# Optimization experiments

Measured on AMD Instinct MI355X. Metric: run time of the kernel, lower is better.

## Reference

```python
import jax, jax.numpy as jnp
import numpy as np

R = 0.15          # ball-query radius (module init arg r)
K = 32            # _MAX_NEIGHBOURS
B, N = 8, 4096


def _ball_query(pos, r, k):
    """Dense ball query. pos: [B,N,3] -> neighbor idx [B,N,K], sorted by distance.
    Slots with fewer than k in-radius neighbors are filled with the query's own
    index (self is always the first neighbor at distance 0), so their
    contribution to (f_i - f_j)^2 is exactly 0 -- matching torch-points-kernels'
    fill-with-first-neighbor behaviour."""
    d2 = jnp.sum((pos[:, :, None, :] - pos[:, None, :, :]) ** 2, axis=-1)  # [B,N,N]
    masked = jnp.where(d2 <= r * r, d2, jnp.inf)
    neg_vals, idx = jax.lax.top_k(-masked, k)          # ascending distance
    valid = neg_vals > -jnp.inf
    self_idx = jnp.arange(pos.shape[1])[None, :, None]
    return jnp.where(valid, idx, self_idx)             # [B,N,K]


def setup_inputs() -> dict:
    key = jax.random.key(0)
    k1, k2 = jax.random.split(key)
    pos = jax.random.uniform(k1, (B, N, 3), dtype=jnp.float32)
    f = jax.random.normal(k2, (B, N), dtype=jnp.float32)
    return {"pos": pos, "f": f}


def reference(pos, f):
    # neighbor indices are non-differentiable (torch gathers with long indices)
    nei_idx = jax.lax.stop_gradient(_ball_query(pos, R, K))      # [B,N,K]
    f_nei = jax.vmap(lambda fb, ib: fb[ib])(f, nei_idx)          # [B,N,K]
    variances = jnp.sum((f[:, :, None] - f_nei) ** 2, axis=-1)   # [B,N]
    return 0.5 * jnp.mean(variances)
```

## Files before the change

### kernel.cpp

```cpp
#include <hip/hip_runtime.h>


#define BQ_K 32
#define CAP 128
#define WPB 4
#define G 6
#define NC (G * G * G)
#define CMAX 64
#define CAPC 512
#define QMAX 64
#define NPTS 4096

__device__ __forceinline__ int cell_coord(float x) {
    int c = (int)(x * (float)G);
    return c < 0 ? 0 : (c > G - 1 ? G - 1 : c);
}

__device__ __forceinline__ float select_sum(float2 e0, float2 e1, int M,
                                            float r2) {
    if (M <= BQ_K) return e0.y + e1.y;
    float lo = 0.0f, hi = r2 * 1.000001f;
    #pragma unroll
    for (int it = 0; it < 12; ++it) {
        const float mid = 0.5f * (lo + hi);
        const int cnt = __popcll(__ballot(e0.x < mid)) +
                        __popcll(__ballot(e1.x < mid));
        if (cnt >= BQ_K) hi = mid; else lo = mid;
    }
    float s = 0.0f;
    if (e0.x < hi) s = e0.y;
    if (e1.x < hi) s += e1.y;
    return s;
}

__global__ void dl_scatter(const float* __restrict__ pos,
                           const float* __restrict__ f,
                           int* __restrict__ cnt, float4* __restrict__ buck,
                           int total) {
    const int t = blockIdx.x * blockDim.x + threadIdx.x;
    if (t >= total) return;
    const int b = t >> 12;
    const float x = pos[3 * (size_t)t + 0];
    const float y = pos[3 * (size_t)t + 1];
    const float z = pos[3 * (size_t)t + 2];
    const int c = (cell_coord(z) * G + cell_coord(y)) * G + cell_coord(x);
    const int cell = b * NC + c;
    const int slot = atomicAdd(&cnt[cell], 1);
    if (slot < CMAX)
        buck[(size_t)cell * CMAX + slot] = make_float4(x, y, z, f[t]);
}

__global__ __launch_bounds__(256) void dl_main(
    const int* __restrict__ cnt, const float4* __restrict__ buck,
    float* __restrict__ out, float r2, float scale)
{
    __shared__ float4 s_cand[CAPC];
    __shared__ float2 s_sel[WPB][CAP];
    __shared__ int    s_q[QMAX];
    __shared__ int    s_ncand, s_nq;
    __shared__ float  s_wsum[WPB];

    const int bc = blockIdx.x;
    const int b  = bc / NC;
    const int c  = bc - b * NC;
    const int cx = c % G, cy = (c / G) % G, cz = c / (G * G);

    const int lane = threadIdx.x & 63;
    const int wave = threadIdx.x >> 6;
    const unsigned long long lmask = (1ULL << lane) - 1ULL;

    if (threadIdx.x == 0) { s_ncand = 0; s_nq = 0; }
    __syncthreads();

    const float lox = cx * (1.0f / G), hix = lox + (1.0f / G);
    const float loy = cy * (1.0f / G), hiy = loy + (1.0f / G);
    const float loz = cz * (1.0f / G), hiz = loz + (1.0f / G);

    for (int n = wave; n < 27; n += WPB) {
        const int nx = cx + (n % 3) - 1;
        const int ny = cy + ((n / 3) % 3) - 1;
        const int nz = cz + (n / 9) - 1;
        if ((unsigned)nx >= (unsigned)G || (unsigned)ny >= (unsigned)G ||
            (unsigned)nz >= (unsigned)G) continue;
        const int cell = b * NC + (nz * G + ny) * G + nx;
        int cc = cnt[cell];
        cc = cc < CMAX ? cc : CMAX;
        const bool have = lane < cc;
        float4 p = make_float4(1e30f, 1e30f, 1e30f, 0.0f);
        if (have) p = buck[(size_t)cell * CMAX + lane];
        const float ddx = fmaxf(fmaxf(lox - p.x, p.x - hix), 0.0f);
        const float ddy = fmaxf(fmaxf(loy - p.y, p.y - hiy), 0.0f);
        const float ddz = fmaxf(fmaxf(loz - p.z, p.z - hiz), 0.0f);
        const float d2c = fmaf(ddx, ddx, fmaf(ddy, ddy, ddz * ddz));
        const bool in = have && (d2c <= r2);
        const unsigned long long m = __ballot(in);
        const int nh = __popcll(m);
        int base = 0;
        if (lane == 0 && nh) base = atomicAdd(&s_ncand, nh);
        base = __shfl(base, 0, 64);
        if (in) {
            const int off = base + __popcll(m & lmask);
            if (off < CAPC) {
                s_cand[off] = p;
                if (n == 13) {
                    const int qs = atomicAdd(&s_nq, 1);
                    if (qs < QMAX) s_q[qs] = off;
                }
            }
        }
    }
    __syncthreads();

    const int ncand = s_ncand < CAPC ? s_ncand : CAPC;
    const int nq    = s_nq < QMAX ? s_nq : QMAX;
    const int ncB   = (ncand + 63) & ~63;

    float2* sel = s_sel[wave];
    float wsum = 0.0f;

    for (int qi = wave; qi < nq; qi += WPB) {
        const float4 qp = s_cand[s_q[qi]];
        const float qx = qp.x, qy = qp.y, qz = qp.z, fi = qp.w;

        int cin = 0;
        for (int basej = 0; basej < ncB; basej += 64) {
            const float4 cd = s_cand[basej + lane];
            const bool valid = (basej + lane) < ncand;
            const float dx = cd.x - qx, dy = cd.y - qy, dz = cd.z - qz;
            const float d2 = fmaf(dx, dx, fmaf(dy, dy, dz * dz));
            const bool inb = valid && (d2 <= r2);
            const unsigned long long mm = __ballot(inb);
            const int off = cin + __popcll(mm & lmask);
            if (inb && off < CAP) {
                const float fd = fi - cd.w;
                sel[off] = make_float2(d2, fd * fd);
            }
            cin += __popcll(mm);
        }
        const int M = cin < CAP ? cin : CAP;

        const float2 e0 = (lane < M) ? sel[lane]
                                     : make_float2(1e30f, 0.0f);
        const float2 e1 = (64 + lane < M) ? sel[64 + lane]
                                          : make_float2(1e30f, 0.0f);
        wsum += select_sum(e0, e1, M, r2);
    }

    for (int o = 32; o > 0; o >>= 1) wsum += __shfl_down(wsum, o, 64);
    if (lane == 0) s_wsum[wave] = wsum;
    __syncthreads();
    if (threadIdx.x == 0) {
        const float bs = s_wsum[0] + s_wsum[1] + s_wsum[2] + s_wsum[3];
        atomicAdd(out, bs * scale);
    }
}

__global__ __launch_bounds__(256) void dl_fallback(
    const float* __restrict__ pos, const float* __restrict__ f,
    float* __restrict__ out, float r2, float scale)
{
    __shared__ float4 s_cand[CAPC];
    __shared__ float2 s_sel[WPB][CAP];
    __shared__ int    s_q[QMAX];
    __shared__ int    s_ncand, s_nq;
    __shared__ float  s_wsum[WPB];

    const int bc = blockIdx.x;
    const int b  = bc / NC;
    const int c  = bc - b * NC;
    const int cx = c % G, cy = (c / G) % G, cz = c / (G * G);
    const int lane = threadIdx.x & 63;
    const int wave = threadIdx.x >> 6;
    const unsigned long long lmask = (1ULL << lane) - 1ULL;

    if (threadIdx.x == 0) { s_ncand = 0; s_nq = 0; }
    __syncthreads();

    const float* posb = pos + (size_t)b * NPTS * 3;
    const float* fb   = f   + (size_t)b * NPTS;
    const float lox = cx * (1.0f / G), hix = lox + (1.0f / G);
    const float loy = cy * (1.0f / G), hiy = loy + (1.0f / G);
    const float loz = cz * (1.0f / G), hiz = loz + (1.0f / G);

    constexpr int per = NPTS / WPB;
    const int wbeg = wave * per;
    for (int j0 = 0; j0 < per; j0 += 64) {
        const int j = wbeg + j0 + lane;
        const float x  = posb[3 * j + 0];
        const float y  = posb[3 * j + 1];
        const float z  = posb[3 * j + 2];
        const float ddx = fmaxf(fmaxf(lox - x, x - hix), 0.0f);
        const float ddy = fmaxf(fmaxf(loy - y, y - hiy), 0.0f);
        const float ddz = fmaxf(fmaxf(loz - z, z - hiz), 0.0f);
        const float d2c = fmaf(ddx, ddx, fmaf(ddy, ddy, ddz * ddz));
        const bool in = (d2c <= r2);
        const unsigned long long m = __ballot(in);
        const int nh = __popcll(m);
        int base = 0;
        if (lane == 0 && nh) base = atomicAdd(&s_ncand, nh);
        base = __shfl(base, 0, 64);
        if (in) {
            const int off = base + __popcll(m & lmask);
            if (off < CAPC) {
                s_cand[off] = make_float4(x, y, z, fb[j]);
                if (cell_coord(x) == cx && cell_coord(y) == cy &&
                    cell_coord(z) == cz) {
                    const int qs = atomicAdd(&s_nq, 1);
                    if (qs < QMAX) s_q[qs] = off;
                }
            }
        }
    }
    __syncthreads();

    const int ncand = s_ncand < CAPC ? s_ncand : CAPC;
    const int nq    = s_nq < QMAX ? s_nq : QMAX;
    const int ncB   = (ncand + 63) & ~63;
    float2* sel = s_sel[wave];
    float wsum = 0.0f;

    for (int qi = wave; qi < nq; qi += WPB) {
        const float4 qp = s_cand[s_q[qi]];
        const float qx = qp.x, qy = qp.y, qz = qp.z, fi = qp.w;
        int cin = 0;
        for (int basej = 0; basej < ncB; basej += 64) {
            const float4 cd = s_cand[basej + lane];
            const bool valid = (basej + lane) < ncand;
            const float dx = cd.x - qx, dy = cd.y - qy, dz = cd.z - qz;
            const float d2 = fmaf(dx, dx, fmaf(dy, dy, dz * dz));
            const bool inb = valid && (d2 <= r2);
            const unsigned long long mm = __ballot(inb);
            const int off = cin + __popcll(mm & lmask);
            if (inb && off < CAP) {
                const float fd = fi - cd.w;
                sel[off] = make_float2(d2, fd * fd);
            }
            cin += __popcll(mm);
        }
        const int M = cin < CAP ? cin : CAP;
        const float2 e0 = (lane < M) ? sel[lane] : make_float2(1e30f, 0.0f);
        const float2 e1 = (64 + lane < M) ? sel[64 + lane]
                                          : make_float2(1e30f, 0.0f);
        wsum += select_sum(e0, e1, M, r2);
    }

    for (int o = 32; o > 0; o >>= 1) wsum += __shfl_down(wsum, o, 64);
    if (lane == 0) s_wsum[wave] = wsum;
    __syncthreads();
    if (threadIdx.x == 0) {
        const float bs = s_wsum[0] + s_wsum[1] + s_wsum[2] + s_wsum[3];
        atomicAdd(out, bs * scale);
    }
}

extern "C" void kernel_launch(void* const* d_in, const int* in_sizes, int n_in,
                              void* d_out, int out_size, void* d_ws, size_t ws_size,
                              hipStream_t stream) {
    const float* pos = (const float*)d_in[0];
    const float* f   = (const float*)d_in[1];
    float* out = (float*)d_out;

    const int B = in_sizes[1] / NPTS;
    const int total = B * NPTS;
    const float r2 = 0.15f * 0.15f;
    const float scale = 0.5f / (float)total;

    hipMemsetAsync(out, 0, sizeof(float), stream);

    const size_t cnt_bytes  = (size_t)B * NC * sizeof(int);
    const size_t buck_bytes = (size_t)B * NC * CMAX * sizeof(float4);
    if (ws_size < cnt_bytes + buck_bytes) {
        dl_fallback<<<B * NC, 256, 0, stream>>>(pos, f, out, r2, scale);
        return;
    }

    int*    cnt  = (int*)d_ws;
    float4* buck = (float4*)((char*)d_ws + cnt_bytes);

    hipMemsetAsync(cnt, 0, cnt_bytes, stream);
    dl_scatter<<<(total + 255) / 256, 256, 0, stream>>>(pos, f, cnt, buck, total);
    dl_main   <<<B * NC, 256, 0, stream>>>(cnt, buck, out, r2, scale);
}
```

Measured before the change: 91.85 us.

## Fuse scatter and main kernels into one cooperative launch with grid sync

Merges the bucket-scatter kernel and the per-cell ball-query kernel into a single cooperative kernel that scatters points, does a grid-wide sync, then runs the main phase. The output zeroing moves into the kernel, which removes one memset and one kernel launch. Grid size is B*NC blocks (1728), and every block must be co-resident, so the launch can fail and drop to the slow fallback. The grid barrier also adds its own sync cost.

```diff
diff --git a/kernel.cpp b/kernel.cpp
--- a/kernel.cpp
+++ b/kernel.cpp
@@ -1,4 +1,7 @@
 #include <hip/hip_runtime.h>
+#include <hip/hip_cooperative_groups.h>
+
+namespace cg = cooperative_groups;
 
 
 #define BQ_K 32
@@ -33,32 +36,35 @@
     return s;
 }
 
-__global__ void dl_scatter(const float* __restrict__ pos,
-                           const float* __restrict__ f,
-                           int* __restrict__ cnt, float4* __restrict__ buck,
-                           int total) {
-    const int t = blockIdx.x * blockDim.x + threadIdx.x;
-    if (t >= total) return;
-    const int b = t >> 12;
-    const float x = pos[3 * (size_t)t + 0];
-    const float y = pos[3 * (size_t)t + 1];
-    const float z = pos[3 * (size_t)t + 2];
-    const int c = (cell_coord(z) * G + cell_coord(y)) * G + cell_coord(x);
-    const int cell = b * NC + c;
-    const int slot = atomicAdd(&cnt[cell], 1);
-    if (slot < CMAX)
-        buck[(size_t)cell * CMAX + slot] = make_float4(x, y, z, f[t]);
-}
-
-__global__ __launch_bounds__(256) void dl_main(
-    const int* __restrict__ cnt, const float4* __restrict__ buck,
-    float* __restrict__ out, float r2, float scale)
+__global__ __launch_bounds__(256) void dl_coop(
+    const float* __restrict__ pos, const float* __restrict__ f,
+    int* __restrict__ cnt, float4* __restrict__ buck,
+    float* __restrict__ out, int total, float r2, float scale)
 {
     __shared__ float4 s_cand[CAPC];
     __shared__ float2 s_sel[WPB][CAP];
     __shared__ int    s_q[QMAX];
     __shared__ int    s_ncand, s_nq;
     __shared__ float  s_wsum[WPB];
+
+    {
+        const int t = blockIdx.x * 256 + threadIdx.x;
+        if (t == 0) out[0] = 0.0f;
+        if (t < total) {
+            const int b = t >> 12;
+            const float x = pos[3 * (size_t)t + 0];
+            const float y = pos[3 * (size_t)t + 1];
+            const float z = pos[3 * (size_t)t + 2];
+            const int c = (cell_coord(z) * G + cell_coord(y)) * G +
+                          cell_coord(x);
+            const int cell = b * NC + c;
+            const int slot = atomicAdd(&cnt[cell], 1);
+            if (slot < CMAX)
+                buck[(size_t)cell * CMAX + slot] =
+                    make_float4(x, y, z, f[t]);
+        }
+    }
+    cg::this_grid().sync();
 
     const int bc = blockIdx.x;
     const int b  = bc / NC;
@@ -261,15 +267,14 @@
     float* out = (float*)d_out;
 
     const int B = in_sizes[1] / NPTS;
-    const int total = B * NPTS;
-    const float r2 = 0.15f * 0.15f;
-    const float scale = 0.5f / (float)total;
-
-    hipMemsetAsync(out, 0, sizeof(float), stream);
+    int total = B * NPTS;
+    float r2 = 0.15f * 0.15f;
+    float scale = 0.5f / (float)total;
 
     const size_t cnt_bytes  = (size_t)B * NC * sizeof(int);
     const size_t buck_bytes = (size_t)B * NC * CMAX * sizeof(float4);
     if (ws_size < cnt_bytes + buck_bytes) {
+        hipMemsetAsync(out, 0, sizeof(float), stream);
         dl_fallback<<<B * NC, 256, 0, stream>>>(pos, f, out, r2, scale);
         return;
     }
@@ -278,6 +283,13 @@
     float4* buck = (float4*)((char*)d_ws + cnt_bytes);
 
     hipMemsetAsync(cnt, 0, cnt_bytes, stream);
-    dl_scatter<<<(total + 255) / 256, 256, 0, stream>>>(pos, f, cnt, buck, total);
-    dl_main   <<<B * NC, 256, 0, stream>>>(cnt, buck, out, r2, scale);
-}
+
+    void* args[] = { (void*)&pos, (void*)&f, (void*)&cnt, (void*)&buck,
+                     (void*)&out, (void*)&total, (void*)&r2, (void*)&scale };
+    const hipError_t err = hipLaunchCooperativeKernel(
+        (const void*)dl_coop, dim3(B * NC), dim3(256), args, 0, stream);
+    if (err != hipSuccess) {
+        hipMemsetAsync(out, 0, sizeof(float), stream);
+        dl_fallback<<<B * NC, 256, 0, stream>>>(pos, f, out, r2, scale);
+    }
+}
```

After: 179.1 us. 95.0% more time.
